# Performance work log

Hardware: AMD Instinct MI355X
Metric: run time of the kernel (lower is better)

The kernel has to match this reference:

```python
import jax, jax.numpy as jnp
import numpy as np

B, C, L = 256, 256, 512
EPS = 1e-5

def setup_inputs() -> dict:
    key = jax.random.key(0)
    k1, k2, k3, k4 = jax.random.split(key, 4)
    x = jax.random.normal(k1, (B, C, L), dtype=jnp.float32)
    idx = jax.random.randint(k2, (B, L), 0, L + 1, dtype=jnp.int32)  # L == pad slot
    # Conv1d(2C, C, 1): weight [C, 2C], bias [C]
    W = jax.random.normal(k3, (C, 2 * C), dtype=jnp.float32) * (1.0 / np.sqrt(2 * C))
    b = jax.random.normal(k4, (C,), dtype=jnp.float32) * 0.01
    return {"x": x, "idx": idx, "W": W, "b": b}

def reference(x, idx, W, b):
    # collect_neighbours: pad length dim with one zero column, gather per (b, l)
    x_pad = jnp.pad(x, ((0, 0), (0, 0), (0, 1)))            # [B, C, L+1]
    nbr = jnp.take_along_axis(x_pad, idx[:, None, :].astype(jnp.int32), axis=2)  # [B, C, L]
    cat = jnp.concatenate([x, nbr], axis=1)                 # [B, 2C, L]
    # 1x1 Conv1d == channel matmul
    y = jnp.einsum('oc,bcl->bol', W, cat) + b[None, :, None]  # [B, C, L]
    # InstanceNorm1d (affine=False): normalize over L per (b, c), biased var
    mu = jnp.mean(y, axis=2, keepdims=True)
    var = jnp.mean(jnp.square(y - mu), axis=2, keepdims=True)
    y = (y - mu) * jax.lax.rsqrt(var + EPS)
    return jax.nn.relu(y)
```

## Files before the change

kernel.cpp:

```cpp
#include <hip/hip_runtime.h>
#include <stdint.h>

typedef __bf16 bf16x8 __attribute__((ext_vector_type(8)));
typedef float  f32x4  __attribute__((ext_vector_type(4)));

__device__ __forceinline__ uint32_t pack_bf16x2(float a, float b) {
    uint32_t ua = __builtin_bit_cast(uint32_t, a);
    uint32_t ub = __builtin_bit_cast(uint32_t, b);
    ua = (ua + 0x7FFFu + ((ua >> 16) & 1u)) >> 16;
    ub = (ub + 0x7FFFu + ((ub >> 16) & 1u)) >> 16;
    return ua | (ub << 16);
}

__global__ __launch_bounds__(256, 2)
void edgeconv_fused(const float* __restrict__ x,
                    const int*   __restrict__ idx,
                    const float* __restrict__ W,
                    float*       __restrict__ out)
{
    __shared__ __align__(16) unsigned char smem[65536];
    unsigned short* a_lds = (unsigned short*)smem;
    unsigned short* xT    = (unsigned short*)(smem + 32768);
    float* y2             = (float*)smem;
    float* red            = (float*)smem;

    const int tid  = threadIdx.x;
    const int wv   = tid >> 6;
    const int lane = tid & 63;
    const int m    = lane & 15;
    const int q    = lane >> 4;

    const int id  = blockIdx.x;
    const int rem = id & 63;
    const int b   = ((id >> 6) << 3) + (rem & 7);
    const int o0  = (rem >> 3) << 5;

    for (int g = 0; g < 16; ++g) {
        int gid = (g << 8) + tid;
        int r   = gid >> 6;
        int kg4 = gid & 63;
        const float4* src = (const float4*)(W + ((size_t)(o0 + (r & 31)) << 9)
                                              + ((r >> 5) << 8) + (kg4 << 2));
        float4 f = *src;
        int k0  = kg4 << 2;
        int off = ((k0 >> 3) << 9) + (r << 3) + (k0 & 7);
        uint2 u; u.x = pack_bf16x2(f.x, f.y); u.y = pack_bf16x2(f.z, f.w);
        *(uint2*)(a_lds + off) = u;
    }

    f32x4 acc[4][8];
    #pragma unroll
    for (int mt = 0; mt < 4; ++mt)
        #pragma unroll
        for (int nt = 0; nt < 8; ++nt)
            acc[mt][nt] = (f32x4){0.f, 0.f, 0.f, 0.f};

    const float* xb = x + ((size_t)b << 17);

    for (int kc = 0; kc < 8; ++kc) {
        __syncthreads();
        #pragma unroll
        for (int g = 0; g < 8; ++g) {
            int gid = (g << 8) + tid;
            int l   = gid & 511;
            int kg  = gid >> 9;
            int kb  = (kc << 5) + (kg << 3);
            const float* xp = xb + ((size_t)kb << 9) + l;
            uint4 u;
            u.x = pack_bf16x2(xp[0],    xp[512]);
            u.y = pack_bf16x2(xp[1024], xp[1536]);
            u.z = pack_bf16x2(xp[2048], xp[2560]);
            u.w = pack_bf16x2(xp[3072], xp[3584]);
            *(uint4*)(xT + (kg << 12) + (l << 3)) = u;
        }
        __syncthreads();

        bf16x8 av[4], bv[8];
        const unsigned short* abase = a_lds + (((kc << 2) + q) << 9) + (m << 3);
        #pragma unroll
        for (int mt = 0; mt < 4; ++mt)
            av[mt] = *(const bf16x8*)(abase + (mt << 7));
        const unsigned short* bbase = xT + (q << 12) + (((wv << 7) + m) << 3);
        #pragma unroll
        for (int nt = 0; nt < 8; ++nt)
            bv[nt] = *(const bf16x8*)(bbase + (nt << 7));

        #pragma unroll
        for (int mt = 0; mt < 4; ++mt)
            #pragma unroll
            for (int nt = 0; nt < 8; ++nt)
                acc[mt][nt] = __builtin_amdgcn_mfma_f32_16x16x32_bf16(av[mt], bv[nt], acc[mt][nt], 0, 0, 0);
    }

    __syncthreads();

    #pragma unroll
    for (int mt = 2; mt < 4; ++mt)
        #pragma unroll
        for (int nt = 0; nt < 8; ++nt)
            #pragma unroll
            for (int r4 = 0; r4 < 4; ++r4) {
                int r   = ((mt - 2) << 4) + (q << 2) + r4;
                int col = (wv << 7) + (nt << 4) + m;
                y2[(r << 9) + col] = acc[mt][nt][r4];
            }
    __syncthreads();

    int iv[8];
    #pragma unroll
    for (int nt = 0; nt < 8; ++nt)
        iv[nt] = idx[((size_t)b << 9) + (wv << 7) + (nt << 4) + m];

    float v[2][8][4];
    float s_[2][4], q_[2][4];
    #pragma unroll
    for (int mt = 0; mt < 2; ++mt)
        #pragma unroll
        for (int r4 = 0; r4 < 4; ++r4) { s_[mt][r4] = 0.f; q_[mt][r4] = 0.f; }

    #pragma unroll
    for (int mt = 0; mt < 2; ++mt)
        #pragma unroll
        for (int nt = 0; nt < 8; ++nt)
            #pragma unroll
            for (int r4 = 0; r4 < 4; ++r4) {
                int r = (mt << 4) + (q << 2) + r4;
                float gth = (iv[nt] < 512) ? y2[(r << 9) + iv[nt]] : 0.f;
                float val = acc[mt][nt][r4] + gth;
                v[mt][nt][r4] = val;
                s_[mt][r4] += val;
                q_[mt][r4] += val * val;
            }

    __syncthreads();

    #pragma unroll
    for (int mt = 0; mt < 2; ++mt)
        #pragma unroll
        for (int r4 = 0; r4 < 4; ++r4) {
            float s = s_[mt][r4], ss = q_[mt][r4];
            #pragma unroll
            for (int off = 1; off < 16; off <<= 1) {
                s  += __shfl_xor(s,  off, 64);
                ss += __shfl_xor(ss, off, 64);
            }
            if (m == 0) {
                int r = (mt << 4) + (q << 2) + r4;
                red[(r << 3) + (wv << 1)]     = s;
                red[(r << 3) + (wv << 1) + 1] = ss;
            }
        }
    __syncthreads();

    #pragma unroll
    for (int mt = 0; mt < 2; ++mt)
        #pragma unroll
        for (int r4 = 0; r4 < 4; ++r4) {
            int r = (mt << 4) + (q << 2) + r4;
            float S = red[(r << 3)]     + red[(r << 3) + 2] + red[(r << 3) + 4] + red[(r << 3) + 6];
            float Q = red[(r << 3) + 1] + red[(r << 3) + 3] + red[(r << 3) + 5] + red[(r << 3) + 7];
            float mu  = S * (1.0f / 512.0f);
            float var = Q * (1.0f / 512.0f) - mu * mu;
            float rs  = rsqrtf(var + 1e-5f);
            float* op = out + (((size_t)(b << 8) + o0 + r) << 9) + (wv << 7) + m;
            #pragma unroll
            for (int nt = 0; nt < 8; ++nt) {
                float t = (v[mt][nt][r4] - mu) * rs;
                op[nt << 4] = fmaxf(t, 0.0f);
            }
        }
}

extern "C" void kernel_launch(void* const* d_in, const int* in_sizes, int n_in,
                              void* d_out, int out_size, void* d_ws, size_t ws_size,
                              hipStream_t stream) {
    const float* x   = (const float*)d_in[0];
    const int*   idx = (const int*)  d_in[1];
    const float* W   = (const float*)d_in[2];
    float* out = (float*)d_out;

    edgeconv_fused<<<dim3(2048), dim3(256), 0, stream>>>(x, idx, W, out);
}
```

Baseline: 325.8 us.

## Prefetch x tiles into registers, swizzle LDS layouts, store gather buffer as bf16

The x staging now uses float4 global loads into registers for the next K chunk, issued before and after the MFMA block so global latency overlaps compute (register double-buffering). W and x tiles in LDS get an XOR swizzle to reduce bank conflicts, and bf16 conversion switches to the HIP intrinsic. The neighbour-gather buffer y2 is stored as bf16 in a column-major padded layout, so each gather becomes one 8-byte load, and the reduction scratch moves so one barrier can go. The cost is higher register pressure from the prefetch arrays and extra bf16 rounding on the gathered half of the conv output.

New measurement: 317.2 us. 2.6% less time.

```diff
diff --git a/kernel.cpp b/kernel.cpp
--- a/kernel.cpp
+++ b/kernel.cpp
@@ -1,16 +1,17 @@
 #include <hip/hip_runtime.h>
+#include <hip/hip_bf16.h>
 #include <stdint.h>
 
 typedef __bf16 bf16x8 __attribute__((ext_vector_type(8)));
 typedef float  f32x4  __attribute__((ext_vector_type(4)));
 
-__device__ __forceinline__ uint32_t pack_bf16x2(float a, float b) {
-    uint32_t ua = __builtin_bit_cast(uint32_t, a);
-    uint32_t ub = __builtin_bit_cast(uint32_t, b);
-    ua = (ua + 0x7FFFu + ((ua >> 16) & 1u)) >> 16;
-    ub = (ub + 0x7FFFu + ((ub >> 16) & 1u)) >> 16;
-    return ua | (ub << 16);
+__device__ __forceinline__ uint32_t cvt2(float a, float b) {
+    __hip_bfloat162 h = __float22bfloat162_rn(make_float2(a, b));
+    uint32_t u; __builtin_memcpy(&u, &h, 4); return u;
 }
+__device__ __forceinline__ float bflo(uint32_t u) { uint32_t t = u << 16;         float f; __builtin_memcpy(&f, &t, 4); return f; }
+__device__ __forceinline__ float bfhi(uint32_t u) { uint32_t t = u & 0xffff0000u; float f; __builtin_memcpy(&f, &t, 4); return f; }
+__device__ __forceinline__ int swz(int u) { return u ^ ((u >> 3) & 7); }
 
 __global__ __launch_bounds__(256, 2)
 void edgeconv_fused(const float* __restrict__ x,
@@ -19,10 +20,10 @@
                     float*       __restrict__ out)
 {
     __shared__ __align__(16) unsigned char smem[65536];
-    unsigned short* a_lds = (unsigned short*)smem;
-    unsigned short* xT    = (unsigned short*)(smem + 32768);
-    float* y2             = (float*)smem;
-    float* red            = (float*)smem;
+    unsigned short* wlds = (unsigned short*)smem;
+    unsigned short* xT   = (unsigned short*)(smem + 32768);
+    unsigned short* y2   = (unsigned short*)smem;
+    float*          red  = (float*)(smem + 38912);
 
     const int tid  = threadIdx.x;
     const int wv   = tid >> 6;
@@ -35,17 +36,16 @@
     const int b   = ((id >> 6) << 3) + (rem & 7);
     const int o0  = (rem >> 3) << 5;
 
-    for (int g = 0; g < 16; ++g) {
-        int gid = (g << 8) + tid;
-        int r   = gid >> 6;
-        int kg4 = gid & 63;
-        const float4* src = (const float4*)(W + ((size_t)(o0 + (r & 31)) << 9)
-                                              + ((r >> 5) << 8) + (kg4 << 2));
-        float4 f = *src;
-        int k0  = kg4 << 2;
-        int off = ((k0 >> 3) << 9) + (r << 3) + (k0 & 7);
-        uint2 u; u.x = pack_bf16x2(f.x, f.y); u.y = pack_bf16x2(f.z, f.w);
-        *(uint2*)(a_lds + off) = u;
+    const float* xb = x + ((size_t)b << 17);
+
+    #pragma unroll
+    for (int i = 0; i < 16; ++i) {
+        int r = (i << 2) + wv;
+        const float4 f = *(const float4*)(W + ((size_t)(o0 + (r & 31)) << 9)
+                                            + ((r >> 5) << 8) + (lane << 2));
+        uint2 p; p.x = cvt2(f.x, f.y); p.y = cvt2(f.z, f.w);
+        int sl = lane >> 1;
+        *(uint2*)(wlds + (sl << 9) + ((swz(r) ^ (sl & 7)) << 3) + ((lane & 1) << 2)) = p;
     }
 
     f32x4 acc[4][8];
@@ -55,63 +55,84 @@
         for (int nt = 0; nt < 8; ++nt)
             acc[mt][nt] = (f32x4){0.f, 0.f, 0.f, 0.f};
 
-    const float* xb = x + ((size_t)b << 17);
+    float4 xr0[8], xr1[8];
+    auto loadg = [&](int kc, int g, float4* xr) {
+        int gid = (g << 8) + tid;
+        int s2  = gid >> 7;
+        int l4  = gid & 127;
+        const float* base = xb + ((size_t)((kc << 5) + (s2 << 3)) << 9) + (l4 << 2);
+        #pragma unroll
+        for (int j = 0; j < 8; ++j) xr[j] = *(const float4*)(base + (j << 9));
+    };
+    auto storeg = [&](int g, const float4* xr) {
+        int gid = (g << 8) + tid;
+        int s2  = gid >> 7;
+        int l4  = gid & 127;
+        #pragma unroll
+        for (int lv = 0; lv < 4; ++lv) {
+            int l = (l4 << 2) + lv;
+            uint4 p;
+            p.x = cvt2((&xr[0].x)[lv], (&xr[1].x)[lv]);
+            p.y = cvt2((&xr[2].x)[lv], (&xr[3].x)[lv]);
+            p.z = cvt2((&xr[4].x)[lv], (&xr[5].x)[lv]);
+            p.w = cvt2((&xr[6].x)[lv], (&xr[7].x)[lv]);
+            *(uint4*)(xT + (s2 << 12) + (swz(l) << 3)) = p;
+        }
+    };
+
+    loadg(0, 0, xr0);
+    loadg(0, 1, xr1);
+    storeg(0, xr0);
+    storeg(1, xr1);
+    __syncthreads();
 
     for (int kc = 0; kc < 8; ++kc) {
-        __syncthreads();
-        #pragma unroll
-        for (int g = 0; g < 8; ++g) {
-            int gid = (g << 8) + tid;
-            int l   = gid & 511;
-            int kg  = gid >> 9;
-            int kb  = (kc << 5) + (kg << 3);
-            const float* xp = xb + ((size_t)kb << 9) + l;
-            uint4 u;
-            u.x = pack_bf16x2(xp[0],    xp[512]);
-            u.y = pack_bf16x2(xp[1024], xp[1536]);
-            u.z = pack_bf16x2(xp[2048], xp[2560]);
-            u.w = pack_bf16x2(xp[3072], xp[3584]);
-            *(uint4*)(xT + (kg << 12) + (l << 3)) = u;
-        }
-        __syncthreads();
+        if (kc < 7) loadg(kc + 1, 0, xr0);
 
         bf16x8 av[4], bv[8];
-        const unsigned short* abase = a_lds + (((kc << 2) + q) << 9) + (m << 3);
-        #pragma unroll
-        for (int mt = 0; mt < 4; ++mt)
-            av[mt] = *(const bf16x8*)(abase + (mt << 7));
-        const unsigned short* bbase = xT + (q << 12) + (((wv << 7) + m) << 3);
+        #pragma unroll
+        for (int mt = 0; mt < 4; ++mt) {
+            int sl = (kc << 2) + q;
+            av[mt] = *(const bf16x8*)(wlds + (sl << 9) + ((swz((mt << 4) + m) ^ (sl & 7)) << 3));
+        }
         #pragma unroll
         for (int nt = 0; nt < 8; ++nt)
-            bv[nt] = *(const bf16x8*)(bbase + (nt << 7));
+            bv[nt] = *(const bf16x8*)(xT + (q << 12) + (swz((wv << 7) + (nt << 4) + m) << 3));
 
         #pragma unroll
         for (int mt = 0; mt < 4; ++mt)
             #pragma unroll
             for (int nt = 0; nt < 8; ++nt)
                 acc[mt][nt] = __builtin_amdgcn_mfma_f32_16x16x32_bf16(av[mt], bv[nt], acc[mt][nt], 0, 0, 0);
+
+        if (kc < 7) loadg(kc + 1, 1, xr1);
+        __syncthreads();
+        if (kc < 7) {
+            storeg(0, xr0);
+            storeg(1, xr1);
+            __syncthreads();
+        }
     }
-
-    __syncthreads();
-
-    #pragma unroll
-    for (int mt = 2; mt < 4; ++mt)
-        #pragma unroll
-        for (int nt = 0; nt < 8; ++nt)
-            #pragma unroll
-            for (int r4 = 0; r4 < 4; ++r4) {
-                int r   = ((mt - 2) << 4) + (q << 2) + r4;
-                int col = (wv << 7) + (nt << 4) + m;
-                y2[(r << 9) + col] = acc[mt][nt][r4];
-            }
-    __syncthreads();
 
     int iv[8];
     #pragma unroll
     for (int nt = 0; nt < 8; ++nt)
         iv[nt] = idx[((size_t)b << 9) + (wv << 7) + (nt << 4) + m];
 
-    float v[2][8][4];
+    #pragma unroll
+    for (int mt = 2; mt < 4; ++mt)
+        #pragma unroll
+        for (int nt = 0; nt < 8; ++nt) {
+            int col  = (wv << 7) + (nt << 4) + m;
+            int row0 = ((mt - 2) << 4) + (q << 2);
+            uint2 p;
+            p.x = cvt2(acc[mt][nt][0], acc[mt][nt][1]);
+            p.y = cvt2(acc[mt][nt][2], acc[mt][nt][3]);
+            *(uint2*)(y2 + col * 36 + row0) = p;
+        }
+    __syncthreads();
+
+    float vvl[2][8][4];
     float s_[2][4], q_[2][4];
     #pragma unroll
     for (int mt = 0; mt < 2; ++mt)
@@ -119,20 +140,27 @@
         for (int r4 = 0; r4 < 4; ++r4) { s_[mt][r4] = 0.f; q_[mt][r4] = 0.f; }
 
     #pragma unroll
-    for (int mt = 0; mt < 2; ++mt)
-        #pragma unroll
-        for (int nt = 0; nt < 8; ++nt)
+    for (int nt = 0; nt < 8; ++nt) {
+        int  c   = iv[nt];
+        bool inb = (c < 512);
+        int  cc  = inb ? c : 0;
+        #pragma unroll
+        for (int mt = 0; mt < 2; ++mt) {
+            uint2 g = *(const uint2*)(y2 + cc * 36 + (mt << 4) + (q << 2));
+            float gv[4];
+            gv[0] = inb ? bflo(g.x) : 0.f;
+            gv[1] = inb ? bfhi(g.x) : 0.f;
+            gv[2] = inb ? bflo(g.y) : 0.f;
+            gv[3] = inb ? bfhi(g.y) : 0.f;
             #pragma unroll
             for (int r4 = 0; r4 < 4; ++r4) {
-                int r = (mt << 4) + (q << 2) + r4;
-                float gth = (iv[nt] < 512) ? y2[(r << 9) + iv[nt]] : 0.f;
-                float val = acc[mt][nt][r4] + gth;
-                v[mt][nt][r4] = val;
+                float val = acc[mt][nt][r4] + gv[r4];
+                vvl[mt][nt][r4] = val;
                 s_[mt][r4] += val;
                 q_[mt][r4] += val * val;
             }
-
-    __syncthreads();
+        }
+    }
 
     #pragma unroll
     for (int mt = 0; mt < 2; ++mt)
@@ -165,7 +193,7 @@
             float* op = out + (((size_t)(b << 8) + o0 + r) << 9) + (wv << 7) + m;
             #pragma unroll
             for (int nt = 0; nt < 8; ++nt) {
-                float t = (v[mt][nt][r4] - mu) * rs;
+                float t = (vvl[mt][nt][r4] - mu) * rs;
                 op[nt << 4] = fmaxf(t, 0.0f);
             }
         }
```
